# Performance work log

Measured on AMD Instinct MI355X. Metric: run time of the kernel, lower is better.

The kernel has to match this reference:

```python
import jax, jax.numpy as jnp
import numpy as np

EPS = 1e-5


def ste_sign(x):
    # Binarize(x) = sign(x) with straight-through identity gradient (torch .data trick)
    return x + jax.lax.stop_gradient(jnp.sign(x) - x)


def conv3x3(x, w):
    # NCHW 3x3 conv, stride 1, zero padding 1 (== ZeroPad2d(1) + 9 shifted views)
    return jax.lax.conv_general_dilated(x, w, (1, 1), [(1, 1), (1, 1)],
                                        dimension_numbers=('NCHW', 'OIHW', 'NCHW'))


def bconv(x, w):
    # Sum of 9 (or 18/36 channel-chunked) shifted binarized 1x1 convs == one binarized 3x3 conv.
    # sign(0)=0 on the zero padding, identical to padding the binarized input.
    return conv3x3(ste_sign(x), ste_sign(w))


def maxpool2(x):
    return jax.lax.reduce_window(x, -jnp.inf, jax.lax.max, (1, 1, 2, 2), (1, 1, 2, 2), 'VALID')


def bn(x, g, b):
    # eval-mode BatchNorm with fresh running stats (mean=0, var=1, eps=1e-5)
    scale = g * jax.lax.rsqrt(jnp.asarray(1.0 + EPS, x.dtype))
    shape = (1, -1) + (1,) * (x.ndim - 2)
    return x * scale.reshape(shape) + b.reshape(shape)


def htanh(x):
    return jnp.clip(x, -1.0, 1.0)


def blinear(x, w, b):
    # BinarizeLinear: in_features != 784 so both input and weight are binarized
    return ste_sign(x) @ ste_sign(w).T + b


def setup_inputs() -> dict:
    key = jax.random.key(0)
    ks = iter(jax.random.split(key, 48))

    def rn(shape, scale=0.05):
        return jax.random.normal(next(ks), shape, dtype=jnp.float32) * scale

    inp = {"x": jax.random.normal(next(ks), (128, 3, 32, 32), dtype=jnp.float32)}
    inp.update(
        w1=rn((128, 3, 3, 3)), c1b=rn((128,)),
        w2=rn((128, 128, 3, 3)),
        w3=rn((256, 128, 3, 3)),
        w4=rn((256, 256, 3, 3)),
        w5=rn((512, 256, 3, 3)),
        w6=rn((512, 512, 3, 3)),
        fw1=rn((1024, 8192)), fb1=rn((1024,)),
        fw2=rn((1024, 1024)), fb2=rn((1024,)),
        fw3=rn((10, 1024)), fb3=rn((10,)),
    )
    for name, c in [("1", 128), ("2", 128), ("3", 256), ("4", 256), ("5", 512), ("6", 512),
                    ("f1", 1024), ("f2", 1024), ("f3", 10)]:
        inp["g" + name] = jax.random.normal(next(ks), (c,), dtype=jnp.float32) * 0.1 + 1.0
        inp["bt" + name] = rn((c,))
    return inp


def reference(x, w1, c1b, w2, w3, w4, w5, w6,
              fw1, fb1, fw2, fb2, fw3, fb3,
              g1, bt1, g2, bt2, g3, bt3, g4, bt4, g5, bt5, g6, bt6,
              gf1, btf1, gf2, btf2, gf3, btf3):
    # block 1: first conv keeps the 3-channel input real, binarizes only the weight
    h = conv3x3(x, ste_sign(w1)) + c1b.reshape(1, -1, 1, 1)
    h = htanh(bn(h, g1, bt1))
    # block 2: 9 shifted binarized 1x1 convs (128->128) -> pool -> BN -> hardtanh
    h = htanh(bn(maxpool2(bconv(h, w2)), g2, bt2))
    # block 3: 9 convs 128->256
    h = htanh(bn(bconv(h, w3), g3, bt3))
    h = htanh(bn(maxpool2(bconv(h, w4)), g4, bt4))
    h = htanh(bn(bconv(h, w5), g5, bt5))
    h = htanh(bn(maxpool2(bconv(h, w6)), g6, bt6))
    h = h.reshape(h.shape[0], -1)  # [B, 512*4*4]
    h = htanh(bn(blinear(h, fw1, fb1), gf1, btf1))
    h = htanh(bn(blinear(h, fw2, fb2), gf2, btf2))
    h = bn(blinear(h, fw3, fb3), gf3, btf3)
    return jax.nn.log_softmax(h, axis=-1)
```

## Files before the change

### kernel.cpp

```cpp
#include <hip/hip_runtime.h>
#include <hip/hip_bf16.h>

using u32 = unsigned int;
using u64 = unsigned long long;
using s8  = signed char;
typedef int i32x4  __attribute__((ext_vector_type(4)));
typedef int i32x16 __attribute__((ext_vector_type(16)));

__device__ __forceinline__ s8 tsign(float t){
  return (t > 0.f) ? (s8)1 : ((t < 0.f) ? (s8)-1 : (s8)0);
}
__device__ __forceinline__ float bn_ts(float z, float sc, float b){
  return __fadd_rn(__fmul_rn(z, sc), b);
}

__global__ void pack_w1_k(const float* __restrict__ w1, u32* __restrict__ wp1){
  int lane = threadIdx.x;
  bool hz = false;
  for (int h = 0; h < 2; h++){
    int co = h*64 + lane;
    u32 a = 0, s = 0, ctlw = 0;
    for (int tap = 0; tap < 9; tap++){
      float v0 = w1[(co*3 + 0)*9 + tap];
      float v1 = w1[(co*3 + 1)*9 + tap];
      float v2 = w1[(co*3 + 2)*9 + tap];
      int b0 = tap*3;
      a |= ((v0 != 0.f) ? 1u : 0u) << b0;     s |= ((v0 > 0.f) ? 1u : 0u) << b0;
      a |= ((v1 != 0.f) ? 1u : 0u) << (b0+1); s |= ((v1 > 0.f) ? 1u : 0u) << (b0+1);
      a |= ((v2 != 0.f) ? 1u : 0u) << (b0+2); s |= ((v2 > 0.f) ? 1u : 0u) << (b0+2);
      hz |= (v0 == 0.f) || (v1 == 0.f) || (v2 == 0.f);
      u32 f = (((v0 > 0.f) == (v1 > 0.f)) ? 1u : 0u)
            | ((v0 < 0.f) ? 2u : 0u)
            | ((v2 < 0.f) ? 4u : 0u);
      ctlw |= f << b0;
    }
    wp1[co*2]   = a;
    wp1[co*2+1] = s;
    wp1[256 + co] = ctlw;
  }
  u64 m = __ballot(hz);
  if (lane == 0) wp1[384] = (m != 0ull) ? 1u : 0u;
}

__global__ __launch_bounds__(256) void mega_k(
    const float* __restrict__ x, const u32* __restrict__ wp1,
    const float* __restrict__ c1b, const float* __restrict__ g1,
    const float* __restrict__ bt1, s8* __restrict__ s1,
    const float* __restrict__ w2, const float* __restrict__ w3,
    const float* __restrict__ w4, const float* __restrict__ w5,
    const float* __restrict__ w6,
    s8* __restrict__ wf2, s8* __restrict__ wf3, s8* __restrict__ wf4,
    s8* __restrict__ wf5, s8* __restrict__ wf6,
    const float* __restrict__ fw1, u32* __restrict__ fw1p,
    const float* __restrict__ fw2, const float* __restrict__ fw3,
    u32* __restrict__ fw2p, u32* __restrict__ fw3p,
    const float* __restrict__ g2, const float* __restrict__ g3,
    const float* __restrict__ g4, const float* __restrict__ g5,
    const float* __restrict__ g6, const float* __restrict__ gf1,
    const float* __restrict__ gf2, const float* __restrict__ gf3,
    float* __restrict__ scb){
  __shared__ char smraw[8192];
  int b = blockIdx.x, tid = threadIdx.x;

  if (b < 2048){
    int lane = tid & 63, wv = tid >> 6;
    int wid = b*4 + wv;
    int coh = wid & 3;
    int chunk = (wid >> 2) & 15;
    int n = wid >> 6;
    int py = lane >> 5, px = lane & 31;
    int y = chunk*2 + py;
    const float* xb = x + (size_t)n*3*1024;
    const float rs = __fdiv_rn(1.0f, __fsqrt_rn((float)(1.0 + 1e-5)));

    float xv[3][9];
    #pragma unroll
    for (int ci = 0; ci < 3; ci++)
      #pragma unroll
      for (int tap = 0; tap < 9; tap++){
        int yy = y + tap/3 - 1, xx = px + tap%3 - 1;
        bool ok = ((unsigned)yy < 32u) && ((unsigned)xx < 32u);
        xv[ci][tap] = ok ? xb[(ci*32 + yy)*32 + xx] : 0.f;
      }
    float pc0[9], pc1[9];
    #pragma unroll
    for (int tap = 0; tap < 9; tap++){
      pc0[tap] = __fadd_rn(xv[0][tap], xv[1][tap]);
      pc1[tap] = __fadd_rn(xv[0][tap], -xv[1][tap]);
    }

    size_t pixbase = (((size_t)n*1024) + y*32 + px)*128 + coh*32;
    bool fallback = (wp1[384] != 0u);

    if (!fallback){
      for (int co4 = 0; co4 < 32; co4 += 4){
        u32 outw = 0;
        #pragma unroll
        for (int j = 0; j < 4; j++){
          int co = coh*32 + co4 + j;
          u32 ctlw = wp1[256 + co];
          float acc = 0.f;
          #pragma unroll
          for (int tap = 0; tap < 9; tap++){
            u32 f = ctlw >> (3*tap);
            float s01 = (f & 1u) ? pc0[tap] : pc1[tap];
            s01 = __uint_as_float(__float_as_uint(s01) ^ ((f & 2u) << 30));
            float t2 = __uint_as_float(__float_as_uint(xv[2][tap]) ^ ((f & 4u) << 29));
            acc = __fadd_rn(acc, __fadd_rn(s01, t2));
          }
          float v = __fadd_rn(acc, c1b[co]);
          float t = bn_ts(v, __fmul_rn(g1[co], rs), bt1[co]);
          outw |= ((u32)(unsigned char)tsign(t)) << (8*j);
        }
        *reinterpret_cast<u32*>(&s1[pixbase + co4]) = outw;
      }
    } else {
      for (int co4 = 0; co4 < 32; co4 += 4){
        u32 outw = 0;
        #pragma unroll
        for (int j = 0; j < 4; j++){
          int co = coh*32 + co4 + j;
          u32 wA = wp1[co*2], wS = wp1[co*2+1];
          float acc = 0.f;
          #pragma unroll
          for (int tap = 0; tap < 9; tap++){
            float pt = 0.f;
            #pragma unroll
            for (int ci = 0; ci < 3; ci++){
              int bit = tap*3 + ci;
              float sg = ((wA >> bit) & 1u) ? (((wS >> bit) & 1u) ? 1.f : -1.f) : 0.f;
              pt = __fadd_rn(pt, __fmul_rn(sg, xv[ci][tap]));
            }
            acc = __fadd_rn(acc, pt);
          }
          float v = __fadd_rn(acc, c1b[co]);
          float t = bn_ts(v, __fmul_rn(g1[co], rs), bt1[co]);
          outw |= ((u32)(unsigned char)tsign(t)) << (8*j);
        }
        *reinterpret_cast<u32*>(&s1[pixbase + co4]) = outw;
      }
    }
  } else if (b < 3712){
    int bb = b - 2048;
    const float* w; s8* wf; int CIN, COUT, co;
    if      (bb < 128) { w=w2; wf=wf2; CIN=128; COUT=128; co=bb; }
    else if (bb < 384) { w=w3; wf=wf3; CIN=128; COUT=256; co=bb-128; }
    else if (bb < 640) { w=w4; wf=wf4; CIN=256; COUT=256; co=bb-384; }
    else if (bb < 1152){ w=w5; wf=wf5; CIN=256; COUT=512; co=bb-640; }
    else               { w=w6; wf=wf6; CIN=512; COUT=512; co=bb-1152; }
    s8* sb = (s8*)smraw;
    int nf = CIN*9;
    const float* wb = w + (size_t)co*nf;
    for (int i = tid; i < nf; i += 256){
      float v = wb[i];
      sb[i] = (v > 0.f) ? (s8)1 : ((v < 0.f) ? (s8)-1 : (s8)0);
    }
    __syncthreads();
    int KK = CIN >> 5, CG = COUT >> 5;
    int cg = co >> 5, llo = co & 31;
    for (int i = tid; i < nf; i += 256){
      int tap = i / CIN, k = i - tap*CIN;
      s8 v = sb[k*9 + tap];
      size_t dst = ((((size_t)tap*KK + (k>>5))*CG + cg)*64
                    + (llo + ((k>>4)&1)*32))*16 + (k&15);
      wf[dst] = v;
    }
  } else if (b < 4736){
    int co = b - 3712;
    unsigned char* sb = (unsigned char*)smraw;
    const float* wb = fw1 + (size_t)co*8192;
    for (int i = tid; i < 8192; i += 256){
      float v = wb[i];
      sb[i] = (unsigned char)(((v != 0.f) ? 2u : 0u) | ((v > 0.f) ? 1u : 0u));
    }
    __syncthreads();
    int kw = tid;
    int px = kw >> 4, cw = kw & 15;
    u32 a = 0, s = 0;
    for (int j = 0; j < 32; j++){
      unsigned char bch = sb[(cw*32 + j)*16 + px];
      a |= (u32)(bch >> 1) << j;
      s |= (u32)(bch & 1u) << j;
    }
    size_t o = ((size_t)kw*1024 + co)*2;
    fw1p[o] = a; fw1p[o+1] = s;
  } else if (b < 5770){
    int bb = b - 4736;
    const float* w; u32* wp; int COUT, co;
    if (bb < 1024){ w = fw2; wp = fw2p; COUT = 1024; co = bb; }
    else          { w = fw3; wp = fw3p; COUT = 10;   co = bb-1024; }
    unsigned char* sb = (unsigned char*)smraw;
    const float* wbp = w + (size_t)co*1024;
    for (int i = tid; i < 1024; i += 256){
      float v = wbp[i];
      sb[i] = (unsigned char)(((v != 0.f) ? 2u : 0u) | ((v > 0.f) ? 1u : 0u));
    }
    __syncthreads();
    for (int kw = tid; kw < 32; kw += 256){
      u32 a = 0, s = 0;
      for (int j = 0; j < 32; j++){
        unsigned char bch = sb[kw*32 + j];
        a |= (u32)(bch >> 1) << j;
        s |= (u32)(bch & 1u) << j;
      }
      size_t o = ((size_t)kw*COUT + co)*2;
      wp[o] = a; wp[o+1] = s;
    }
  } else {
    int i = (b - 5770)*256 + tid;
    const float rs = __fdiv_rn(1.0f, __fsqrt_rn((float)(1.0 + 1e-5)));
    float v;
    if      (i < 128)  v = g1[i];
    else if (i < 256)  v = g2[i-128];
    else if (i < 512)  v = g3[i-256];
    else if (i < 768)  v = g4[i-512];
    else if (i < 1280) v = g5[i-768];
    else if (i < 1792) v = g6[i-1280];
    else if (i < 2816) v = gf1[i-1792];
    else if (i < 3840) v = gf2[i-2816];
    else if (i < 3850) v = gf3[i-3840];
    else return;
    scb[i] = __fmul_rn(v, rs);
  }
}

template<int CIN, int COUT, int H, int W, int POOL, int BITOUT>
__global__ __launch_bounds__(256) void bconv_l(
    const s8* __restrict__ A, const s8* __restrict__ WF,
    const float* __restrict__ sc, const float* __restrict__ bt,
    s8* __restrict__ O, u32* __restrict__ OB){
  constexpr int KK = CIN/32, CG = COUT/32, CGB = 2;
  constexpr int XT = (W >= 16) ? 16 : 8;
  constexpr int YT = 32 / XT;
  constexpr int TPR = W / XT;
  constexpr int TROWS = H / YT;
  constexpr int NMT = 128*TROWS*TPR;
  constexpr int HO = POOL ? H/2 : H, WO = POOL ? W/2 : W;
  constexpr int RY = (XT == 16) ? 8 : 4;
  constexpr int TAPB = KK*CGB*1024;
  __shared__ s8 Bsh[2][TAPB];

  int tid = threadIdx.x, lane = tid & 63, wv = tid >> 6;
  int wid = blockIdx.x*4 + wv;
  int mt = wid % NMT; int cb = wid / NMT;
  int tx = mt % TPR; int r0 = mt / TPR;
  int ty = r0 % TROWS; int n = r0 / TROWS;
  int y0 = ty*YT, x0 = tx*XT;
  int p = lane & 31;
  int py = p / XT, px = p % XT;
  int y = y0 + py, x = x0 + px;
  int kh = lane >> 5;
  const s8* An = A + (size_t)n*H*W*CIN;

  auto stage = [&](int buf, int tap){
    const s8* src0 = WF + (((size_t)tap*KK)*CG + (size_t)cb*CGB)*1024;
    #pragma unroll
    for (int j = 0; j < TAPB/(256*16); j++){
      int byte = (tid + j*256)*16;
      int kk = byte / (CGB*1024);
      int rem = byte - kk*(CGB*1024);
      *reinterpret_cast<uint4*>(&Bsh[buf][byte]) =
        *reinterpret_cast<const uint4*>(src0 + (size_t)kk*CG*1024 + rem);
    }
  };

  i32x16 acc0 = {0,0,0,0,0,0,0,0,0,0,0,0,0,0,0,0};
  i32x16 acc1 = acc0;

  stage(0, 0);
  __syncthreads();
  int buf = 0;
  #pragma unroll
  for (int tap = 0; tap < 9; tap++){
    if (tap < 8) stage(buf^1, tap+1);
    int dy = tap/3 - 1, dx = tap%3 - 1;
    int sy = y + dy, sx = x + dx;
    bool ok = ((unsigned)sy < (unsigned)H) && ((unsigned)sx < (unsigned)W);
    const s8* ap = An + ((size_t)sy*W + sx)*CIN + kh*16;
    #pragma unroll
    for (int kk = 0; kk < KK; kk++){
      i32x4 av = {0,0,0,0};
      if (ok) av = *reinterpret_cast<const i32x4*>(ap + kk*32);
      i32x4 b0 = *reinterpret_cast<const i32x4*>(&Bsh[buf][(kk*CGB+0)*1024 + lane*16]);
      i32x4 b1 = *reinterpret_cast<const i32x4*>(&Bsh[buf][(kk*CGB+1)*1024 + lane*16]);
      acc0 = __builtin_amdgcn_mfma_i32_32x32x32_i8(av, b0, acc0, 0, 0, 0);
      acc1 = __builtin_amdgcn_mfma_i32_32x32x32_i8(av, b1, acc1, 0, 0, 0);
    }
    __syncthreads();
    buf ^= 1;
  }

  auto epi = [&](const i32x16& acc, int cgb){
    int co = (cb*CGB + cgb)*32 + (lane & 31);
    float ss = sc[co], bb = bt[co];
    if (POOL){
      #pragma unroll
      for (int q = 0; q < 4; q++){
        int rr = (q&1)*2 + (q>>1)*((XT == 16) ? 4 : 8);
        int z = max(max(acc[rr], acc[rr+1]), max(acc[rr+RY], acc[rr+RY+1]));
        float t = bn_ts((float)z, ss, bb);
        if (!BITOUT){
          int pb = (rr&3) + 8*(rr>>2) + 4*kh;
          int yy = y0 + pb/XT, xx2 = x0 + pb%XT;
          int oy = yy >> 1, ox = xx2 >> 1;
          O[(((size_t)n*HO + oy)*WO + ox)*COUT + co] = tsign(t);
        } else {
          u64 mP = __ballot(t > 0.f);
          u64 mN = __ballot(t < 0.f);
          if (lane == 0){
            u64 mA = mP | mN;
            int cw = cb*CGB + cgb;
            int pb0 = (rr&3) + 8*(rr>>2);
            int yy0 = y0 + pb0/XT, xx0 = x0 + pb0%XT;
            int p0 = (yy0>>1)*4 + (xx0>>1);
            int pb1 = pb0 + 4;
            int yy1 = y0 + pb1/XT, xx1 = x0 + pb1%XT;
            int p1 = (yy1>>1)*4 + (xx1>>1);
            size_t o0 = ((size_t)n*256 + p0*16 + cw)*2;
            size_t o1 = ((size_t)n*256 + p1*16 + cw)*2;
            OB[o0]   = (u32)mA;       OB[o0+1] = (u32)mP;
            OB[o1]   = (u32)(mA>>32); OB[o1+1] = (u32)(mP>>32);
          }
        }
      }
    } else {
      #pragma unroll
      for (int rr = 0; rr < 16; rr++){
        int pb = (rr&3) + 8*(rr>>2) + 4*kh;
        int yy = y0 + pb/XT, xx2 = x0 + pb%XT;
        float t = bn_ts((float)acc[rr], ss, bb);
        O[(((size_t)n*H + yy)*W + xx2)*COUT + co] = tsign(t);
      }
    }
  };
  epi(acc0, 0); epi(acc1, 1);
}

template<int KW>
__global__ __launch_bounds__(256) void fcb_k(
    const u32* __restrict__ A, const u32* __restrict__ Wp,
    const float* __restrict__ fb,
    const float* __restrict__ sc, const float* __restrict__ bt,
    u32* __restrict__ Op){
  int tid = threadIdx.x; int lane = tid & 63; int wv = tid >> 6;
  int wid = blockIdx.x*4 + wv;
  int og = wid & 15; int n = wid >> 4;
  int o = og*64 + lane;
  const uint2* a = reinterpret_cast<const uint2*>(&A[(size_t)n*KW*2]);
  int z = 0;
  #pragma unroll 8
  for (int kw = 0; kw < KW; kw++){
    uint2 av = a[kw];
    uint2 wv_ = reinterpret_cast<const uint2*>(Wp)[kw*1024 + o];
    u32 v = av.x & wv_.x;
    u32 d = v & (av.y ^ wv_.y);
    z += __popc(v) - 2*__popc(d);
  }
  float vv = __fadd_rn((float)z, fb[o]);
  float t = bn_ts(vv, sc[o], bt[o]);
  u64 mP = __ballot(t > 0.f);
  u64 mN = __ballot(t < 0.f);
  if (lane == 0){
    int ob = (n*32 + og*2)*2;
    Op[ob]   = (u32)(mP | mN);
    Op[ob+1] = (u32)mP;
    Op[ob+2] = (u32)((mP | mN) >> 32);
    Op[ob+3] = (u32)(mP >> 32);
  }
}

__global__ void fc3_k(const u32* __restrict__ A, const u32* __restrict__ Wp,
                      const float* __restrict__ fb,
                      const float* __restrict__ sc,
                      const float* __restrict__ bt,
                      float* __restrict__ out){
  int n = blockIdx.x; int lane = threadIdx.x;
  __shared__ double ls[10];
  double t = 0.0;
  if (lane < 10){
    const uint2* a = reinterpret_cast<const uint2*>(&A[(size_t)n*32*2]);
    int z = 0;
    for (int kw = 0; kw < 32; kw++){
      uint2 av = a[kw];
      uint2 wv_ = reinterpret_cast<const uint2*>(Wp)[kw*10 + lane];
      u32 v = av.x & wv_.x;
      u32 d = v & (av.y ^ wv_.y);
      z += __popc(v) - 2*__popc(d);
    }
    float vv = __fadd_rn((float)z, fb[lane]);
    float tf = bn_ts(vv, sc[lane], bt[lane]);
    t = (double)tf;
    ls[lane] = t;
  }
  __syncthreads();
  if (lane < 10){
    double m = -1e300;
    for (int j = 0; j < 10; j++) m = fmax(m, ls[j]);
    double sum = 0.0;
    for (int j = 0; j < 10; j++) sum += exp(ls[j] - m);
    double r = t - m - log(sum);
    out[n*10 + lane] = (float)r;
  }
}

extern "C" void kernel_launch(void* const* d_in, const int* in_sizes, int n_in,
                              void* d_out, int out_size, void* d_ws, size_t ws_size,
                              hipStream_t stream){
  auto f = [&](int i){ return (const float*)d_in[i]; };
  const float *x  = f(0),  *w1 = f(1),  *c1b = f(2),
    *w2 = f(3),  *w3 = f(4),  *w4 = f(5),  *w5 = f(6),  *w6 = f(7),
    *fw1 = f(8), *fb1 = f(9), *fw2 = f(10), *fb2 = f(11),
    *fw3 = f(12), *fb3 = f(13),
    *g1 = f(14), *bt1 = f(15), *g2 = f(16), *bt2 = f(17),
    *g3 = f(18), *bt3 = f(19), *g4 = f(20), *bt4 = f(21),
    *g5 = f(22), *bt5 = f(23), *g6 = f(24), *bt6 = f(25),
    *gf1 = f(26), *btf1 = f(27), *gf2 = f(28), *btf2 = f(29),
    *gf3 = f(30), *btf3 = f(31);

  char* base = (char*)d_ws;
  size_t off = 0;
  auto alloc = [&](size_t bytes){ char* p = base + off; off += (bytes + 255) & ~(size_t)255; return p; };
  s8* poolA = (s8*)alloc(128ull*32*32*128);
  s8* poolB = (s8*)alloc(128ull*16*16*128);
  s8 *s1 = poolA, *s3 = poolA, *s5 = poolA;
  s8 *s2 = poolB, *s4 = poolB;
  s8 *wf2 = (s8*)alloc(9ull*128*128), *wf3 = (s8*)alloc(9ull*128*256),
     *wf4 = (s8*)alloc(9ull*256*256), *wf5 = (s8*)alloc(9ull*256*512),
     *wf6 = (s8*)alloc(9ull*512*512);
  u32 *wp1  = (u32*)alloc(385*4);
  float* scb = (float*)alloc(3850*4);
  u32 *fw1p = (u32*)alloc(2ull*256*1024*4), *fw2p = (u32*)alloc(2ull*32*1024*4),
      *fw3p = (u32*)alloc(2ull*32*10*4);
  u32 *s6p  = (u32*)alloc(2ull*128*256*4);
  u32 *sf1  = (u32*)alloc(2ull*128*32*4), *sf2 = (u32*)alloc(2ull*128*32*4);

  float *sc2 = scb+128, *sc3 = scb+256, *sc4 = scb+512,
        *sc5 = scb+768, *sc6 = scb+1280, *scf1 = scb+1792, *scf2 = scb+2816,
        *scf3 = scb+3840;

  pack_w1_k<<<1, 64, 0, stream>>>(w1, wp1);
  mega_k<<<5786, 256, 0, stream>>>(
      x, wp1, c1b, g1, bt1, s1,
      w2, w3, w4, w5, w6, wf2, wf3, wf4, wf5, wf6,
      fw1, fw1p, fw2, fw3, fw2p, fw3p,
      g2, g3, g4, g5, g6, gf1, gf2, gf3, scb);

  bconv_l<128,128,32,32,1,0><<<2048, 256, 0, stream>>>(s1, wf2, sc2, bt2, s2, nullptr);
  bconv_l<128,256,16,16,0,0><<<1024, 256, 0, stream>>>(s2, wf3, sc3, bt3, s3, nullptr);
  bconv_l<256,256,16,16,1,0><<<1024, 256, 0, stream>>>(s3, wf4, sc4, bt4, s4, nullptr);
  bconv_l<256,512, 8, 8,0,0><<< 512, 256, 0, stream>>>(s4, wf5, sc5, bt5, s5, nullptr);
  bconv_l<512,512, 8, 8,1,1><<< 512, 256, 0, stream>>>(s5, wf6, sc6, bt6, nullptr, s6p);
  fcb_k<256><<<(128*16)/4, 256, 0, stream>>>(s6p, fw1p, fb1, scf1, btf1, sf1);
  fcb_k<32><<<(128*16)/4,  256, 0, stream>>>(sf1, fw2p, fb2, scf2, btf2, sf2);
  fc3_k<<<128, 64, 0, stream>>>(sf2, fw3p, fb3, scf3, btf3, (float*)d_out);
}
```

Baseline: 287.8 us.

## Restructure first conv, widen later conv blocks, fuse FC layers into one kernel

New measurement: 346.0 us. 20.2% more time.

```diff
diff --git a/kernel.cpp b/kernel.cpp
--- a/kernel.cpp
+++ b/kernel.cpp
@@ -73,73 +73,78 @@
     const float* xb = x + (size_t)n*3*1024;
     const float rs = __fdiv_rn(1.0f, __fsqrt_rn((float)(1.0 + 1e-5)));
 
-    float xv[3][9];
-    #pragma unroll
-    for (int ci = 0; ci < 3; ci++)
+    u32 ctl[32];
+    #pragma unroll
+    for (int j = 0; j < 32; j++) ctl[j] = wp1[256 + coh*32 + j];
+
+    float acc[32];
+    #pragma unroll
+    for (int j = 0; j < 32; j++) acc[j] = 0.f;
+
+    bool fallback = (wp1[384] != 0u);
+
+    if (!fallback){
       #pragma unroll
       for (int tap = 0; tap < 9; tap++){
-        int yy = y + tap/3 - 1, xx = px + tap%3 - 1;
-        bool ok = ((unsigned)yy < 32u) && ((unsigned)xx < 32u);
-        xv[ci][tap] = ok ? xb[(ci*32 + yy)*32 + xx] : 0.f;
-      }
-    float pc0[9], pc1[9];
-    #pragma unroll
-    for (int tap = 0; tap < 9; tap++){
-      pc0[tap] = __fadd_rn(xv[0][tap], xv[1][tap]);
-      pc1[tap] = __fadd_rn(xv[0][tap], -xv[1][tap]);
+        int iy = y + tap/3 - 1, ix = px + tap%3 - 1;
+        bool ok = ((unsigned)iy < 32u) && ((unsigned)ix < 32u);
+        float x0 = ok ? xb[(0*32 + iy)*32 + ix] : 0.f;
+        float x1 = ok ? xb[(1*32 + iy)*32 + ix + 0*0 + 0] : 0.f;
+        float x2 = ok ? xb[(2*32 + iy)*32 + ix] : 0.f;
+        float pc0 = __fadd_rn(x0, x1);
+        float pc1 = __fadd_rn(x0, -x1);
+        #pragma unroll
+        for (int j = 0; j < 32; j++){
+          u32 f = ctl[j] >> (3*tap);
+          float s01 = (f & 1u) ? pc0 : pc1;
+          s01 = __uint_as_float(__float_as_uint(s01) ^ ((f & 2u) << 30));
+          float t2 = __uint_as_float(__float_as_uint(x2) ^ ((f & 4u) << 29));
+          acc[j] = __fadd_rn(acc[j], __fadd_rn(s01, t2));
+        }
+      }
+    } else {
+      #pragma unroll
+      for (int tap = 0; tap < 9; tap++){
+        int iy = y + tap/3 - 1, ix = px + tap%3 - 1;
+        bool ok = ((unsigned)iy < 32u) && ((unsigned)ix < 32u);
+        float xv0 = ok ? xb[(0*32 + iy)*32 + ix] : 0.f;
+        float xv1 = ok ? xb[(1*32 + iy)*32 + ix] : 0.f;
+        float xv2 = ok ? xb[(2*32 + iy)*32 + ix] : 0.f;
+        #pragma unroll
+        for (int j = 0; j < 32; j++){
+          int co = coh*32 + j;
+          u32 wA = wp1[co*2], wS = wp1[co*2+1];
+          int bit = tap*3;
+          float pt = 0.f;
+          float sg0 = ((wA >> bit) & 1u) ? (((wS >> bit) & 1u) ? 1.f : -1.f) : 0.f;
+          pt = __fadd_rn(pt, __fmul_rn(sg0, xv0));
+          float sg1 = ((wA >> (bit+1)) & 1u) ? (((wS >> (bit+1)) & 1u) ? 1.f : -1.f) : 0.f;
+          pt = __fadd_rn(pt, __fmul_rn(sg1, xv1));
+          float sg2 = ((wA >> (bit+2)) & 1u) ? (((wS >> (bit+2)) & 1u) ? 1.f : -1.f) : 0.f;
+          pt = __fadd_rn(pt, __fmul_rn(sg2, xv2));
+          acc[j] = __fadd_rn(acc[j], pt);
+        }
+      }
     }
 
     size_t pixbase = (((size_t)n*1024) + y*32 + px)*128 + coh*32;
-    bool fallback = (wp1[384] != 0u);
-
-    if (!fallback){
-      for (int co4 = 0; co4 < 32; co4 += 4){
-        u32 outw = 0;
-        #pragma unroll
-        for (int j = 0; j < 4; j++){
-          int co = coh*32 + co4 + j;
-          u32 ctlw = wp1[256 + co];
-          float acc = 0.f;
-          #pragma unroll
-          for (int tap = 0; tap < 9; tap++){
-            u32 f = ctlw >> (3*tap);
-            float s01 = (f & 1u) ? pc0[tap] : pc1[tap];
-            s01 = __uint_as_float(__float_as_uint(s01) ^ ((f & 2u) << 30));
-            float t2 = __uint_as_float(__float_as_uint(xv[2][tap]) ^ ((f & 4u) << 29));
-            acc = __fadd_rn(acc, __fadd_rn(s01, t2));
-          }
-          float v = __fadd_rn(acc, c1b[co]);
-          float t = bn_ts(v, __fmul_rn(g1[co], rs), bt1[co]);
-          outw |= ((u32)(unsigned char)tsign(t)) << (8*j);
-        }
-        *reinterpret_cast<u32*>(&s1[pixbase + co4]) = outw;
-      }
-    } else {
-      for (int co4 = 0; co4 < 32; co4 += 4){
-        u32 outw = 0;
-        #pragma unroll
-        for (int j = 0; j < 4; j++){
-          int co = coh*32 + co4 + j;
-          u32 wA = wp1[co*2], wS = wp1[co*2+1];
-          float acc = 0.f;
-          #pragma unroll
-          for (int tap = 0; tap < 9; tap++){
-            float pt = 0.f;
-            #pragma unroll
-            for (int ci = 0; ci < 3; ci++){
-              int bit = tap*3 + ci;
-              float sg = ((wA >> bit) & 1u) ? (((wS >> bit) & 1u) ? 1.f : -1.f) : 0.f;
-              pt = __fadd_rn(pt, __fmul_rn(sg, xv[ci][tap]));
-            }
-            acc = __fadd_rn(acc, pt);
-          }
-          float v = __fadd_rn(acc, c1b[co]);
-          float t = bn_ts(v, __fmul_rn(g1[co], rs), bt1[co]);
-          outw |= ((u32)(unsigned char)tsign(t)) << (8*j);
-        }
-        *reinterpret_cast<u32*>(&s1[pixbase + co4]) = outw;
-      }
-    }
+    u32 ow[8];
+    #pragma unroll
+    for (int co4 = 0; co4 < 32; co4 += 4){
+      u32 outw = 0;
+      #pragma unroll
+      for (int j = 0; j < 4; j++){
+        int co = coh*32 + co4 + j;
+        float v = __fadd_rn(acc[co4 + j], c1b[co]);
+        float t = bn_ts(v, __fmul_rn(g1[co], rs), bt1[co]);
+        outw |= ((u32)(unsigned char)tsign(t)) << (8*j);
+      }
+      ow[co4/4] = outw;
+    }
+    uint4 st0 = { ow[0], ow[1], ow[2], ow[3] };
+    uint4 st1 = { ow[4], ow[5], ow[6], ow[7] };
+    *reinterpret_cast<uint4*>(&s1[pixbase])      = st0;
+    *reinterpret_cast<uint4*>(&s1[pixbase + 16]) = st1;
   } else if (b < 3712){
     int bb = b - 2048;
     const float* w; s8* wf; int CIN, COUT, co;
@@ -224,8 +229,8 @@
   }
 }
 
-template<int CIN, int COUT, int H, int W, int POOL, int BITOUT>
-__global__ __launch_bounds__(256) void bconv_l(
+template<int CIN, int COUT, int H, int W, int POOL, int BITOUT, int WPB>
+__global__ __launch_bounds__(WPB*64) void bconv_l(
     const s8* __restrict__ A, const s8* __restrict__ WF,
     const float* __restrict__ sc, const float* __restrict__ bt,
     s8* __restrict__ O, u32* __restrict__ OB){
@@ -238,10 +243,11 @@
   constexpr int HO = POOL ? H/2 : H, WO = POOL ? W/2 : W;
   constexpr int RY = (XT == 16) ? 8 : 4;
   constexpr int TAPB = KK*CGB*1024;
+  constexpr int NT = WPB*64;
   __shared__ s8 Bsh[2][TAPB];
 
   int tid = threadIdx.x, lane = tid & 63, wv = tid >> 6;
-  int wid = blockIdx.x*4 + wv;
+  int wid = blockIdx.x*WPB + wv;
   int mt = wid % NMT; int cb = wid / NMT;
   int tx = mt % TPR; int r0 = mt / TPR;
   int ty = r0 % TROWS; int n = r0 / TROWS;
@@ -255,8 +261,8 @@
   auto stage = [&](int buf, int tap){
     const s8* src0 = WF + (((size_t)tap*KK)*CG + (size_t)cb*CGB)*1024;
     #pragma unroll
-    for (int j = 0; j < TAPB/(256*16); j++){
-      int byte = (tid + j*256)*16;
+    for (int j = 0; j < TAPB/(NT*16); j++){
+      int byte = (tid + j*NT)*16;
       int kk = byte / (CGB*1024);
       int rem = byte - kk*(CGB*1024);
       *reinterpret_cast<uint4*>(&Bsh[buf][byte]) =
@@ -336,70 +342,93 @@
   epi(acc0, 0); epi(acc1, 1);
 }
 
-template<int KW>
-__global__ __launch_bounds__(256) void fcb_k(
-    const u32* __restrict__ A, const u32* __restrict__ Wp,
-    const float* __restrict__ fb,
-    const float* __restrict__ sc, const float* __restrict__ bt,
-    u32* __restrict__ Op){
-  int tid = threadIdx.x; int lane = tid & 63; int wv = tid >> 6;
-  int wid = blockIdx.x*4 + wv;
-  int og = wid & 15; int n = wid >> 4;
-  int o = og*64 + lane;
-  const uint2* a = reinterpret_cast<const uint2*>(&A[(size_t)n*KW*2]);
-  int z = 0;
-  #pragma unroll 8
-  for (int kw = 0; kw < KW; kw++){
-    uint2 av = a[kw];
-    uint2 wv_ = reinterpret_cast<const uint2*>(Wp)[kw*1024 + o];
-    u32 v = av.x & wv_.x;
-    u32 d = v & (av.y ^ wv_.y);
-    z += __popc(v) - 2*__popc(d);
-  }
-  float vv = __fadd_rn((float)z, fb[o]);
-  float t = bn_ts(vv, sc[o], bt[o]);
-  u64 mP = __ballot(t > 0.f);
-  u64 mN = __ballot(t < 0.f);
-  if (lane == 0){
-    int ob = (n*32 + og*2)*2;
-    Op[ob]   = (u32)(mP | mN);
-    Op[ob+1] = (u32)mP;
-    Op[ob+2] = (u32)((mP | mN) >> 32);
-    Op[ob+3] = (u32)(mP >> 32);
-  }
-}
-
-__global__ void fc3_k(const u32* __restrict__ A, const u32* __restrict__ Wp,
-                      const float* __restrict__ fb,
-                      const float* __restrict__ sc,
-                      const float* __restrict__ bt,
-                      float* __restrict__ out){
-  int n = blockIdx.x; int lane = threadIdx.x;
+__global__ __launch_bounds__(256) void fc_all_k(
+    const u32* __restrict__ A0, const u32* __restrict__ W1,
+    const float* __restrict__ fb1, const float* __restrict__ sc1f,
+    const float* __restrict__ bt1f,
+    const u32* __restrict__ W2, const float* __restrict__ fb2,
+    const float* __restrict__ sc2f, const float* __restrict__ bt2f,
+    const u32* __restrict__ W3, const float* __restrict__ fb3,
+    const float* __restrict__ sc3f, const float* __restrict__ bt3f,
+    float* __restrict__ out){
+  int n = blockIdx.x, tid = threadIdx.x;
+  __shared__ u32 Ash[512];
+  __shared__ s8 tern[1024];
   __shared__ double ls[10];
-  double t = 0.0;
-  if (lane < 10){
-    const uint2* a = reinterpret_cast<const uint2*>(&A[(size_t)n*32*2]);
+  for (int i = tid; i < 512; i += 256) Ash[i] = A0[(size_t)n*512 + i];
+  __syncthreads();
+  int z1[4] = {0,0,0,0};
+  for (int kw = 0; kw < 256; kw++){
+    u32 aA = Ash[kw*2], aS = Ash[kw*2+1];
+    #pragma unroll
+    for (int q = 0; q < 4; q++){
+      int o = tid + q*256;
+      uint2 w = reinterpret_cast<const uint2*>(W1)[kw*1024 + o];
+      u32 v = aA & w.x; u32 d = v & (aS ^ w.y);
+      z1[q] += __popc(v) - 2*__popc(d);
+    }
+  }
+  #pragma unroll
+  for (int q = 0; q < 4; q++){
+    int o = tid + q*256;
+    float vv = __fadd_rn((float)z1[q], fb1[o]);
+    tern[o] = tsign(bn_ts(vv, sc1f[o], bt1f[o]));
+  }
+  __syncthreads();
+  if (tid < 32){
+    u32 a = 0, s = 0;
+    for (int j = 0; j < 32; j++){
+      s8 v = tern[tid*32 + j];
+      a |= (u32)(v != 0) << j; s |= (u32)(v > 0) << j;
+    }
+    Ash[tid*2] = a; Ash[tid*2+1] = s;
+  }
+  __syncthreads();
+  int z2[4] = {0,0,0,0};
+  for (int kw = 0; kw < 32; kw++){
+    u32 aA = Ash[kw*2], aS = Ash[kw*2+1];
+    #pragma unroll
+    for (int q = 0; q < 4; q++){
+      int o = tid + q*256;
+      uint2 w = reinterpret_cast<const uint2*>(W2)[kw*1024 + o];
+      u32 v = aA & w.x; u32 d = v & (aS ^ w.y);
+      z2[q] += __popc(v) - 2*__popc(d);
+    }
+  }
+  #pragma unroll
+  for (int q = 0; q < 4; q++){
+    int o = tid + q*256;
+    float vv = __fadd_rn((float)z2[q], fb2[o]);
+    tern[o] = tsign(bn_ts(vv, sc2f[o], bt2f[o]));
+  }
+  __syncthreads();
+  if (tid < 32){
+    u32 a = 0, s = 0;
+    for (int j = 0; j < 32; j++){
+      s8 v = tern[tid*32 + j];
+      a |= (u32)(v != 0) << j; s |= (u32)(v > 0) << j;
+    }
+    Ash[tid*2] = a; Ash[tid*2+1] = s;
+  }
+  __syncthreads();
+  if (tid < 10){
     int z = 0;
     for (int kw = 0; kw < 32; kw++){
-      uint2 av = a[kw];
-      uint2 wv_ = reinterpret_cast<const uint2*>(Wp)[kw*10 + lane];
-      u32 v = av.x & wv_.x;
-      u32 d = v & (av.y ^ wv_.y);
+      u32 aA = Ash[kw*2], aS = Ash[kw*2+1];
+      uint2 w = reinterpret_cast<const uint2*>(W3)[kw*10 + tid];
+      u32 v = aA & w.x; u32 d = v & (aS ^ w.y);
       z += __popc(v) - 2*__popc(d);
     }
-    float vv = __fadd_rn((float)z, fb[lane]);
-    float tf = bn_ts(vv, sc[lane], bt[lane]);
-    t = (double)tf;
-    ls[lane] = t;
-  }
-  __syncthreads();
-  if (lane < 10){
+    float vv = __fadd_rn((float)z, fb3[tid]);
+    ls[tid] = (double)bn_ts(vv, sc3f[tid], bt3f[tid]);
+  }
+  __syncthreads();
+  if (tid < 10){
     double m = -1e300;
     for (int j = 0; j < 10; j++) m = fmax(m, ls[j]);
     double sum = 0.0;
     for (int j = 0; j < 10; j++) sum += exp(ls[j] - m);
-    double r = t - m - log(sum);
-    out[n*10 + lane] = (float)r;
+    out[n*10 + tid] = (float)(ls[tid] - m - log(sum));
   }
 }
 
@@ -432,7 +461,6 @@
   u32 *fw1p = (u32*)alloc(2ull*256*1024*4), *fw2p = (u32*)alloc(2ull*32*1024*4),
       *fw3p = (u32*)alloc(2ull*32*10*4);
   u32 *s6p  = (u32*)alloc(2ull*128*256*4);
-  u32 *sf1  = (u32*)alloc(2ull*128*32*4), *sf2 = (u32*)alloc(2ull*128*32*4);
 
   float *sc2 = scb+128, *sc3 = scb+256, *sc4 = scb+512,
         *sc5 = scb+768, *sc6 = scb+1280, *scf1 = scb+1792, *scf2 = scb+2816,
@@ -445,12 +473,12 @@
       fw1, fw1p, fw2, fw3, fw2p, fw3p,
       g2, g3, g4, g5, g6, gf1, gf2, gf3, scb);
 
-  bconv_l<128,128,32,32,1,0><<<2048, 256, 0, stream>>>(s1, wf2, sc2, bt2, s2, nullptr);
-  bconv_l<128,256,16,16,0,0><<<1024, 256, 0, stream>>>(s2, wf3, sc3, bt3, s3, nullptr);
-  bconv_l<256,256,16,16,1,0><<<1024, 256, 0, stream>>>(s3, wf4, sc4, bt4, s4, nullptr);
-  bconv_l<256,512, 8, 8,0,0><<< 512, 256, 0, stream>>>(s4, wf5, sc5, bt5, s5, nullptr);
-  bconv_l<512,512, 8, 8,1,1><<< 512, 256, 0, stream>>>(s5, wf6, sc6, bt6, nullptr, s6p);
-  fcb_k<256><<<(128*16)/4, 256, 0, stream>>>(s6p, fw1p, fb1, scf1, btf1, sf1);
-  fcb_k<32><<<(128*16)/4,  256, 0, stream>>>(sf1, fw2p, fb2, scf2, btf2, sf2);
-  fc3_k<<<128, 64, 0, stream>>>(sf2, fw3p, fb3, scf3, btf3, (float*)d_out);
-}
+  bconv_l<128,128,32,32,1,0,4><<<2048, 256, 0, stream>>>(s1, wf2, sc2, bt2, s2, nullptr);
+  bconv_l<128,256,16,16,0,0,4><<<1024, 256, 0, stream>>>(s2, wf3, sc3, bt3, s3, nullptr);
+  bconv_l<256,256,16,16,1,0,8><<< 512, 512, 0, stream>>>(s3, wf4, sc4, bt4, s4, nullptr);
+  bconv_l<256,512, 8, 8,0,0,8><<< 256, 512, 0, stream>>>(s4, wf5, sc5, bt5, s5, nullptr);
+  bconv_l<512,512, 8, 8,1,1,8><<< 256, 512, 0, stream>>>(s5, wf6, sc6, bt6, nullptr, s6p);
+  fc_all_k<<<128, 256, 0, stream>>>(s6p, fw1p, fb1, scf1, btf1,
+                                    fw2p, fb2, scf2, btf2,
+                                    fw3p, fb3, scf3, btf3, (float*)d_out);
+}
```
